# Performance work log

Measured on AMD Instinct MI355X. Metric: run time of the kernel, lower is better.

Reference implementation:

```python
import jax, jax.numpy as jnp
import numpy as np

B, NB, TB = 16, 16, 256          # batch, num cache blocks, tokens per block
EMBED, NH, NKV, HD = 2048, 32, 8, 64  # embed dim, query heads, kv heads, head dim
LAST_OFFSET = 192                # valid length of the final cached block


def setup_inputs() -> dict:
    key = jax.random.key(0)
    ks = jax.random.split(key, 7)
    w = 0.02
    return {
        "x": jax.random.normal(ks[0], (B, 1, EMBED), jnp.float32),
        "blocks_k": jax.random.normal(ks[1], (NB, B, NKV, TB, HD), jnp.float32),
        "blocks_v": jax.random.normal(ks[2], (NB, B, NKV, TB, HD), jnp.float32),
        "Wq": jax.random.normal(ks[3], (EMBED, EMBED), jnp.float32) * w,
        "Wk": jax.random.normal(ks[4], (NKV * HD, EMBED), jnp.float32) * w,
        "Wv": jax.random.normal(ks[5], (NKV * HD, EMBED), jnp.float32) * w,
        "Wo": jax.random.normal(ks[6], (EMBED, EMBED), jnp.float32) * w,
        "last_offset": LAST_OFFSET,
    }


def reference(x, blocks_k, blocks_v, Wq, Wk, Wv, Wo, last_offset):
    # Decode step (T == 1) of GQA MultiHeadAttention with paged/blockwise KV cache.
    Bx, T, C = x.shape                      # T == 1
    nb, _, hkv, tb, hd = blocks_k.shape
    nh = C // hd
    g = nh // hkv                           # GQA group size
    scale = hd ** -0.5

    # Projections (nn.Linear with bias=False => x @ W.T)
    q = (x @ Wq.T).reshape(Bx, hkv, g, hd)          # (B, H_kv, g, D); T==1 folded
    k_cur = (x @ Wk.T).reshape(Bx, hkv, 1, hd)      # (B, H_kv, 1, D)
    v_cur = (x @ Wv.T).reshape(Bx, hkv, 1, hd)

    # Gather cached blocks into a contiguous view: (nb,B,Hkv,tb,D) -> (B,Hkv,nb*tb,D)
    Kc = jnp.transpose(blocks_k, (1, 2, 0, 3, 4)).reshape(Bx, hkv, nb * tb, hd)
    Vc = jnp.transpose(blocks_v, (1, 2, 0, 3, 4)).reshape(Bx, hkv, nb * tb, hd)
    K = jnp.concatenate([Kc, k_cur], axis=2)        # (B, H_kv, nb*tb+1, D)
    V = jnp.concatenate([Vc, v_cur], axis=2)

    # Valid positions: all full blocks, last cached block truncated to last_offset,
    # plus the current token. Equivalent to the streaming softmax over blocks.
    pos = jnp.arange(nb * tb)
    mask = jnp.concatenate([pos < (nb - 1) * tb + last_offset,
                            jnp.ones((1,), dtype=bool)])

    # GQA scores without materializing expanded KV heads
    scores = jnp.einsum('bhgd,bhkd->bhgk', q, K) * scale   # (B, H_kv, g, L)
    scores = jnp.where(mask, scores, jnp.finfo(scores.dtype).min)
    probs = jax.nn.softmax(scores, axis=-1)
    o = jnp.einsum('bhgk,bhkd->bhgd', probs, V)             # (B, H_kv, g, D)

    atten = o.reshape(Bx, 1, C)                              # heads -> channels
    out = atten @ Wo.T                                       # (B, 1, C)
    return out
```

## Files before the change

### kernel.cpp

```cpp
#include <hip/hip_runtime.h>
#include <cstdint>
#include <cstddef>

#define BATCH 16
#define NBLK 16
#define TB 256
#define EMBED 2048
#define NKV 8
#define GQ 4
#define HD 64
#define NQROWS 3072
#define TTOT 4096
#define QSCALE 0.18033688011112042f
#define NEGBIG (-1e30f)

#define OFF_PARTM  49152
#define OFF_PARTS  81920
#define OFF_CMB    114688
#define OFF_PARTO  116736
#define OFF_ATTEN  641024
#define OFF_S      673792

__device__ __forceinline__ float dot4(float4 a, float4 b) {
  return a.x * b.x + a.y * b.y + a.z * b.z + a.w * b.w;
}

template <int CTRL>
__device__ __forceinline__ float dpp_add(float x) {
  return x + __int_as_float(
                 __builtin_amdgcn_mov_dpp(__float_as_int(x), CTRL, 0xF, 0xF, true));
}

#define PROJ_RPB 4
__global__ __launch_bounds__(256) void proj_kernel(
    const float* __restrict__ x, const float* __restrict__ Wq,
    const float* __restrict__ Wk, const float* __restrict__ Wv,
    float* __restrict__ proj) {
  int tid = threadIdx.x;
  int bb = tid & 15, kc = tid >> 4;
  int row0 = blockIdx.x * PROJ_RPB;
  const float* xp = x + (size_t)bb * EMBED + kc * 128;
  const float* wr[PROJ_RPB];
#pragma unroll
  for (int r = 0; r < PROJ_RPB; ++r) {
    int row = row0 + r;
    wr[r] = (row < 2048 ? Wq + (size_t)row * EMBED
             : row < 2560 ? Wk + (size_t)(row - 2048) * EMBED
                          : Wv + (size_t)(row - 2560) * EMBED) + kc * 128;
  }
  float a[PROJ_RPB] = {0.f, 0.f, 0.f, 0.f};
#pragma unroll
  for (int k = 0; k < 128; k += 8) {
    float4 x0 = *reinterpret_cast<const float4*>(xp + k);
    float4 x1 = *reinterpret_cast<const float4*>(xp + k + 4);
#pragma unroll
    for (int r = 0; r < PROJ_RPB; ++r) {
      float4 w0 = *reinterpret_cast<const float4*>(wr[r] + k);
      float4 w1 = *reinterpret_cast<const float4*>(wr[r] + k + 4);
      a[r] += dot4(w0, x0) + dot4(w1, x1);
    }
  }
  int w = tid >> 6, lane = tid & 63;
  __shared__ float red[4][PROJ_RPB][16];
#pragma unroll
  for (int r = 0; r < PROJ_RPB; ++r) {
    float s = a[r];
    s += __shfl_xor(s, 16);
    s += __shfl_xor(s, 32);
    if (lane < 16) red[w][r][lane] = s;
  }
  __syncthreads();
  if (tid < 16 * PROJ_RPB) {
    int r = tid >> 4, b2 = tid & 15;
    float v = red[0][r][b2] + red[1][r][b2] + red[2][r][b2] + red[3][r][b2];
    proj[(size_t)b2 * NQROWS + row0 + r] = v;
  }
}

__global__ __launch_bounds__(256) void score_kernel(
    const float* __restrict__ blocks_k, const float* __restrict__ proj,
    const int* __restrict__ last_offset, float* __restrict__ sbuf,
    float* __restrict__ part_m, float* __restrict__ part_s) {
  int nb = blockIdx.x, b = blockIdx.y, h = blockIdx.z;
  int tid = threadIdx.x;
  int w = tid >> 6, lane = tid & 63;
  int tq = lane >> 2;
  int qd = lane & 3;
  int valid = (nb == NBLK - 1) ? last_offset[0] : TB;

  float4 qv[GQ][4];
  const float* qbase = proj + (size_t)b * NQROWS + h * GQ * HD + qd * 16;
#pragma unroll
  for (int gi = 0; gi < GQ; ++gi)
#pragma unroll
    for (int j = 0; j < 4; ++j)
      qv[gi][j] = *reinterpret_cast<const float4*>(qbase + gi * HD + j * 4);

  const float* kg = blocks_k + (((size_t)nb * BATCH + b) * NKV + h) * (TB * HD);
  float* sout = sbuf + ((size_t)(b * NKV + h)) * (TTOT * GQ) +
                (size_t)(nb * TB + w * 64) * GQ;

  float m[GQ], sm[GQ];
#pragma unroll
  for (int gi = 0; gi < GQ; ++gi) { m[gi] = NEGBIG; sm[gi] = 0.f; }

#pragma unroll
  for (int i = 0; i < 4; ++i) {
    int tl = w * 64 + i * 16 + tq;
    const float* kp = kg + (size_t)tl * HD + qd * 16;
    float4 k0 = *reinterpret_cast<const float4*>(kp);
    float4 k1 = *reinterpret_cast<const float4*>(kp + 4);
    float4 k2 = *reinterpret_cast<const float4*>(kp + 8);
    float4 k3 = *reinterpret_cast<const float4*>(kp + 12);
    float s[GQ];
#pragma unroll
    for (int gi = 0; gi < GQ; ++gi) {
      s[gi] = dot4(qv[gi][0], k0) + dot4(qv[gi][1], k1) +
              dot4(qv[gi][2], k2) + dot4(qv[gi][3], k3);
      s[gi] = dpp_add<0xB1>(s[gi]);
      s[gi] = dpp_add<0x4E>(s[gi]);
      s[gi] = (tl < valid) ? s[gi] : NEGBIG;
    }
#pragma unroll
    for (int gi = 0; gi < GQ; ++gi) {
      float im = s[gi];
#pragma unroll
      for (int mask = 4; mask < 64; mask <<= 1) im = fmaxf(im, __shfl_xor(im, mask));
      float mn = fmaxf(m[gi], im);
      float c = exp2f((m[gi] - mn) * QSCALE);
      float e = exp2f((s[gi] - mn) * QSCALE);
      float es = e;
#pragma unroll
      for (int mask = 4; mask < 64; mask <<= 1) es += __shfl_xor(es, mask);
      sm[gi] = sm[gi] * c + es;
      m[gi] = mn;
    }
    float v01 = (qd & 1) ? s[1] : s[0];
    float v23 = (qd & 1) ? s[3] : s[2];
    float v = (qd & 2) ? v23 : v01;
    sout[(size_t)(i * 16) * GQ + lane] = v;
  }

  if (lane == 0) {
#pragma unroll
    for (int gi = 0; gi < GQ; ++gi) {
      size_t wi = ((size_t)(b * NKV + h) * GQ + gi);
      part_m[wi * 64 + nb * 4 + w] = m[gi];
      part_s[wi * 64 + nb * 4 + w] = sm[gi];
    }
  }
}

__global__ __launch_bounds__(256) void combine_kernel(
    const float* __restrict__ proj, const float* __restrict__ part_m,
    const float* __restrict__ part_s, float4* __restrict__ cmb) {
  int tid = threadIdx.x;
  int wi = blockIdx.x * 4 + (tid >> 6);
  int lane = tid & 63;
  int b = wi >> 5;
  int h = (wi >> 2) & 7;
  int gi = wi & 3;

  float pm = part_m[(size_t)wi * 64 + lane];
  float ps = part_s[(size_t)wi * 64 + lane];

  float qd = proj[(size_t)b * NQROWS + (h * GQ + gi) * HD + lane];
  float kd = proj[(size_t)b * NQROWS + 2048 + h * HD + lane];
  float sp = qd * kd;
#pragma unroll
  for (int mask = 1; mask < 64; mask <<= 1) sp += __shfl_xor(sp, mask);

  float M = pm;
#pragma unroll
  for (int mask = 1; mask < 64; mask <<= 1) M = fmaxf(M, __shfl_xor(M, mask));
  M = fmaxf(M, sp);

  float contrib = ps * exp2f((pm - M) * QSCALE);
#pragma unroll
  for (int mask = 1; mask < 64; mask <<= 1) contrib += __shfl_xor(contrib, mask);
  float p_cur = exp2f((sp - M) * QSCALE);
  float T = contrib + p_cur;
  if (lane == 0) cmb[wi] = make_float4(M, p_cur, 1.f / T, 0.f);
}

__global__ __launch_bounds__(256) void pv_kernel(
    const float* __restrict__ blocks_v, const float* __restrict__ sbuf,
    const float4* __restrict__ cmb, float* __restrict__ part_o) {
  int nb = blockIdx.x, b = blockIdx.y, h = blockIdx.z;
  int tid = threadIdx.x;
  int w = tid >> 6, lane = tid & 63;
  int sub = lane >> 4, dl = (lane & 15) * 4;

  const float* vg = blocks_v + (((size_t)nb * BATCH + b) * NKV + h) * (TB * HD);
  const float* sg = sbuf + ((size_t)(b * NKV + h)) * (TTOT * GQ) +
                    (size_t)(nb * TB) * GQ;

  float Mv[GQ];
#pragma unroll
  for (int gi = 0; gi < GQ; ++gi)
    Mv[gi] = cmb[(size_t)(b * NKV + h) * GQ + gi].x;

  float4 acc[GQ];
#pragma unroll
  for (int gi = 0; gi < GQ; ++gi) acc[gi] = make_float4(0.f, 0.f, 0.f, 0.f);

#pragma unroll
  for (int i = 0; i < 4; ++i) {
    float4 v4[4], s4[4];
#pragma unroll
    for (int j = 0; j < 4; ++j) {
      int tl = w * 64 + i * 16 + j * 4 + sub;
      v4[j] = *reinterpret_cast<const float4*>(vg + (size_t)tl * HD + dl);
      s4[j] = *reinterpret_cast<const float4*>(sg + (size_t)tl * GQ);
    }
#pragma unroll
    for (int j = 0; j < 4; ++j) {
      float p0 = exp2f((s4[j].x - Mv[0]) * QSCALE);
      float p1 = exp2f((s4[j].y - Mv[1]) * QSCALE);
      float p2 = exp2f((s4[j].z - Mv[2]) * QSCALE);
      float p3 = exp2f((s4[j].w - Mv[3]) * QSCALE);
      acc[0].x += p0 * v4[j].x; acc[0].y += p0 * v4[j].y;
      acc[0].z += p0 * v4[j].z; acc[0].w += p0 * v4[j].w;
      acc[1].x += p1 * v4[j].x; acc[1].y += p1 * v4[j].y;
      acc[1].z += p1 * v4[j].z; acc[1].w += p1 * v4[j].w;
      acc[2].x += p2 * v4[j].x; acc[2].y += p2 * v4[j].y;
      acc[2].z += p2 * v4[j].z; acc[2].w += p2 * v4[j].w;
      acc[3].x += p3 * v4[j].x; acc[3].y += p3 * v4[j].y;
      acc[3].z += p3 * v4[j].z; acc[3].w += p3 * v4[j].w;
    }
  }

#pragma unroll
  for (int mask = 16; mask <= 32; mask <<= 1) {
#pragma unroll
    for (int gi = 0; gi < GQ; ++gi) {
      acc[gi].x += __shfl_xor(acc[gi].x, mask);
      acc[gi].y += __shfl_xor(acc[gi].y, mask);
      acc[gi].z += __shfl_xor(acc[gi].z, mask);
      acc[gi].w += __shfl_xor(acc[gi].w, mask);
    }
  }

  __shared__ float lds_o[4][GQ][HD];
  if (lane < 16) {
#pragma unroll
    for (int gi = 0; gi < GQ; ++gi)
      *reinterpret_cast<float4*>(&lds_o[w][gi][dl]) = acc[gi];
  }
  __syncthreads();
  if (w == 0) {
    int d = lane;
#pragma unroll
    for (int gi = 0; gi < GQ; ++gi) {
      float o = lds_o[0][gi][d] + lds_o[1][gi][d] + lds_o[2][gi][d] + lds_o[3][gi][d];
      part_o[(((size_t)(b * NKV + h) * GQ + gi) * NBLK + nb) * HD + d] = o;
    }
  }
}

__global__ __launch_bounds__(256) void reduce_kernel(
    const float* __restrict__ proj, const float* __restrict__ part_o,
    const float4* __restrict__ cmb, float* __restrict__ atten) {
  int tid = threadIdx.x;
  int wi = blockIdx.x * 4 + (tid >> 6);
  int lane = tid & 63;
  int b = wi >> 5;
  int h = (wi >> 2) & 7;
  int gi = wi & 3;
  size_t pidx = (size_t)wi * NBLK;

  float4 c4 = cmb[wi];
  float vd = proj[(size_t)b * NQROWS + 2560 + h * HD + lane];
  float o = c4.y * vd;
#pragma unroll
  for (int nb = 0; nb < NBLK; ++nb) o += part_o[(pidx + nb) * HD + lane];
  atten[(size_t)b * EMBED + (h * GQ + gi) * HD + lane] = o * c4.z;
}

#define OUT_RPB 4
__global__ __launch_bounds__(256) void out_kernel(
    const float* __restrict__ atten, const float* __restrict__ Wo,
    float* __restrict__ out) {
  int tid = threadIdx.x;
  int bb = tid & 15, kc = tid >> 4;
  int row0 = blockIdx.x * OUT_RPB;
  const float* xp = atten + (size_t)bb * EMBED + kc * 128;
  float a[OUT_RPB] = {0.f, 0.f, 0.f, 0.f};
#pragma unroll
  for (int k = 0; k < 128; k += 8) {
    float4 x0 = *reinterpret_cast<const float4*>(xp + k);
    float4 x1 = *reinterpret_cast<const float4*>(xp + k + 4);
#pragma unroll
    for (int r = 0; r < OUT_RPB; ++r) {
      const float* wp = Wo + (size_t)(row0 + r) * EMBED + kc * 128;
      float4 w0 = *reinterpret_cast<const float4*>(wp + k);
      float4 w1 = *reinterpret_cast<const float4*>(wp + k + 4);
      a[r] += dot4(w0, x0) + dot4(w1, x1);
    }
  }
  int w = tid >> 6, lane = tid & 63;
  __shared__ float red[4][OUT_RPB][16];
#pragma unroll
  for (int r = 0; r < OUT_RPB; ++r) {
    float s = a[r];
    s += __shfl_xor(s, 16);
    s += __shfl_xor(s, 32);
    if (lane < 16) red[w][r][lane] = s;
  }
  __syncthreads();
  if (tid < 16 * OUT_RPB) {
    int r = tid >> 4, b2 = tid & 15;
    float v = red[0][r][b2] + red[1][r][b2] + red[2][r][b2] + red[3][r][b2];
    out[(size_t)b2 * EMBED + row0 + r] = v;
  }
}

extern "C" void kernel_launch(void* const* d_in, const int* in_sizes, int n_in,
                              void* d_out, int out_size, void* d_ws, size_t ws_size,
                              hipStream_t stream) {
  const float* x = (const float*)d_in[0];
  const float* bk = (const float*)d_in[1];
  const float* bv = (const float*)d_in[2];
  const float* Wq = (const float*)d_in[3];
  const float* Wk = (const float*)d_in[4];
  const float* Wv = (const float*)d_in[5];
  const float* Wo = (const float*)d_in[6];
  const int* lo = (const int*)d_in[7];

  float* ws = (float*)d_ws;
  float* proj = ws;
  float* part_m = ws + OFF_PARTM;
  float* part_s = ws + OFF_PARTS;
  float4* cmb = (float4*)(ws + OFF_CMB);
  float* part_o = ws + OFF_PARTO;
  float* atten = ws + OFF_ATTEN;
  float* sbuf = ws + OFF_S;
  float* out = (float*)d_out;

  proj_kernel<<<NQROWS / PROJ_RPB, 256, 0, stream>>>(x, Wq, Wk, Wv, proj);
  score_kernel<<<dim3(NBLK, BATCH, NKV), 256, 0, stream>>>(bk, proj, lo, sbuf,
                                                           part_m, part_s);
  combine_kernel<<<(BATCH * NKV * GQ) / 4, 256, 0, stream>>>(proj, part_m,
                                                             part_s, cmb);
  pv_kernel<<<dim3(NBLK, BATCH, NKV), 256, 0, stream>>>(bv, sbuf, cmb, part_o);
  reduce_kernel<<<(BATCH * NKV * GQ) / 4, 256, 0, stream>>>(proj, part_o, cmb,
                                                            atten);
  out_kernel<<<EMBED / OUT_RPB, 256, 0, stream>>>(atten, Wo, out);
}
```

Measured before the change: 141.6 us.

## Split each KV block across two workgroups and batch loads upfront

The score and PV kernels now launch twice as many workgroups, each covering half of a 256-token cache block. Each wave handles 32 tokens and issues all of its K/V and score loads before a sched_barrier, which gives more memory parallelism per wave. The score kernel drops the per-iteration online-softmax rescaling and computes one max/sum per wave. The partial max/sum and partial output buffers double in size, so the combine and reduce kernels read and sum twice as many partials, and the workspace offsets grow to fit.

```diff
diff --git a/kernel.cpp b/kernel.cpp
--- a/kernel.cpp
+++ b/kernel.cpp
@@ -15,11 +15,11 @@
 #define NEGBIG (-1e30f)
 
 #define OFF_PARTM  49152
-#define OFF_PARTS  81920
-#define OFF_CMB    114688
-#define OFF_PARTO  116736
-#define OFF_ATTEN  641024
-#define OFF_S      673792
+#define OFF_PARTS  114688
+#define OFF_CMB    180224
+#define OFF_PARTO  182272
+#define OFF_ATTEN  1230848
+#define OFF_S      1263616
 
 __device__ __forceinline__ float dot4(float4 a, float4 b) {
   return a.x * b.x + a.y * b.y + a.z * b.z + a.w * b.w;
@@ -81,12 +81,14 @@
     const float* __restrict__ blocks_k, const float* __restrict__ proj,
     const int* __restrict__ last_offset, float* __restrict__ sbuf,
     float* __restrict__ part_m, float* __restrict__ part_s) {
-  int nb = blockIdx.x, b = blockIdx.y, h = blockIdx.z;
+  int tb2 = blockIdx.x, b = blockIdx.y, h = blockIdx.z;
+  int nb = tb2 >> 1;
   int tid = threadIdx.x;
   int w = tid >> 6, lane = tid & 63;
   int tq = lane >> 2;
   int qd = lane & 3;
   int valid = (nb == NBLK - 1) ? last_offset[0] : TB;
+  int tok0 = (tb2 & 1) * 128 + w * 32;
 
   float4 qv[GQ][4];
   const float* qbase = proj + (size_t)b * NQROWS + h * GQ * HD + qd * 16;
@@ -97,56 +99,52 @@
       qv[gi][j] = *reinterpret_cast<const float4*>(qbase + gi * HD + j * 4);
 
   const float* kg = blocks_k + (((size_t)nb * BATCH + b) * NKV + h) * (TB * HD);
+
+  float4 kr[2][4];
+#pragma unroll
+  for (int i = 0; i < 2; ++i) {
+    const float* kp = kg + (size_t)(tok0 + i * 16 + tq) * HD + qd * 16;
+#pragma unroll
+    for (int j = 0; j < 4; ++j)
+      kr[i][j] = *reinterpret_cast<const float4*>(kp + j * 4);
+  }
+  __builtin_amdgcn_sched_barrier(0);
+
+  float s[2][GQ];
+#pragma unroll
+  for (int i = 0; i < 2; ++i) {
+#pragma unroll
+    for (int gi = 0; gi < GQ; ++gi) {
+      float t = dot4(qv[gi][0], kr[i][0]) + dot4(qv[gi][1], kr[i][1]) +
+                dot4(qv[gi][2], kr[i][2]) + dot4(qv[gi][3], kr[i][3]);
+      t = dpp_add<0xB1>(t);
+      t = dpp_add<0x4E>(t);
+      s[i][gi] = (tok0 + i * 16 + tq) < valid ? t : NEGBIG;
+    }
+  }
+
   float* sout = sbuf + ((size_t)(b * NKV + h)) * (TTOT * GQ) +
-                (size_t)(nb * TB + w * 64) * GQ;
-
-  float m[GQ], sm[GQ];
-#pragma unroll
-  for (int gi = 0; gi < GQ; ++gi) { m[gi] = NEGBIG; sm[gi] = 0.f; }
-
-#pragma unroll
-  for (int i = 0; i < 4; ++i) {
-    int tl = w * 64 + i * 16 + tq;
-    const float* kp = kg + (size_t)tl * HD + qd * 16;
-    float4 k0 = *reinterpret_cast<const float4*>(kp);
-    float4 k1 = *reinterpret_cast<const float4*>(kp + 4);
-    float4 k2 = *reinterpret_cast<const float4*>(kp + 8);
-    float4 k3 = *reinterpret_cast<const float4*>(kp + 12);
-    float s[GQ];
-#pragma unroll
-    for (int gi = 0; gi < GQ; ++gi) {
-      s[gi] = dot4(qv[gi][0], k0) + dot4(qv[gi][1], k1) +
-              dot4(qv[gi][2], k2) + dot4(qv[gi][3], k3);
-      s[gi] = dpp_add<0xB1>(s[gi]);
-      s[gi] = dpp_add<0x4E>(s[gi]);
-      s[gi] = (tl < valid) ? s[gi] : NEGBIG;
-    }
-#pragma unroll
-    for (int gi = 0; gi < GQ; ++gi) {
-      float im = s[gi];
-#pragma unroll
-      for (int mask = 4; mask < 64; mask <<= 1) im = fmaxf(im, __shfl_xor(im, mask));
-      float mn = fmaxf(m[gi], im);
-      float c = exp2f((m[gi] - mn) * QSCALE);
-      float e = exp2f((s[gi] - mn) * QSCALE);
-      float es = e;
-#pragma unroll
-      for (int mask = 4; mask < 64; mask <<= 1) es += __shfl_xor(es, mask);
-      sm[gi] = sm[gi] * c + es;
-      m[gi] = mn;
-    }
-    float v01 = (qd & 1) ? s[1] : s[0];
-    float v23 = (qd & 1) ? s[3] : s[2];
-    float v = (qd & 2) ? v23 : v01;
-    sout[(size_t)(i * 16) * GQ + lane] = v;
-  }
-
-  if (lane == 0) {
-#pragma unroll
-    for (int gi = 0; gi < GQ; ++gi) {
-      size_t wi = ((size_t)(b * NKV + h) * GQ + gi);
-      part_m[wi * 64 + nb * 4 + w] = m[gi];
-      part_s[wi * 64 + nb * 4 + w] = sm[gi];
+                (size_t)(nb * TB + tok0) * GQ;
+#pragma unroll
+  for (int i = 0; i < 2; ++i) {
+    float v01 = (qd & 1) ? s[i][1] : s[i][0];
+    float v23 = (qd & 1) ? s[i][3] : s[i][2];
+    sout[(size_t)(i * 16) * GQ + lane] = (qd & 2) ? v23 : v01;
+  }
+
+#pragma unroll
+  for (int gi = 0; gi < GQ; ++gi) {
+    float mx = fmaxf(s[0][gi], s[1][gi]);
+#pragma unroll
+    for (int mask = 4; mask < 64; mask <<= 1)
+      mx = fmaxf(mx, __shfl_xor(mx, mask));
+    float sm = exp2f((s[0][gi] - mx) * QSCALE) + exp2f((s[1][gi] - mx) * QSCALE);
+#pragma unroll
+    for (int mask = 4; mask < 64; mask <<= 1) sm += __shfl_xor(sm, mask);
+    if (lane == 0) {
+      size_t wi = (size_t)(b * NKV + h) * GQ + gi;
+      part_m[wi * 128 + tb2 * 4 + w] = mx;
+      part_s[wi * 128 + tb2 * 4 + w] = sm;
     }
   }
 }
@@ -161,8 +159,10 @@
   int h = (wi >> 2) & 7;
   int gi = wi & 3;
 
-  float pm = part_m[(size_t)wi * 64 + lane];
-  float ps = part_s[(size_t)wi * 64 + lane];
+  float pm_a = part_m[(size_t)wi * 128 + lane];
+  float pm_b = part_m[(size_t)wi * 128 + 64 + lane];
+  float ps_a = part_s[(size_t)wi * 128 + lane];
+  float ps_b = part_s[(size_t)wi * 128 + 64 + lane];
 
   float qd = proj[(size_t)b * NQROWS + (h * GQ + gi) * HD + lane];
   float kd = proj[(size_t)b * NQROWS + 2048 + h * HD + lane];
@@ -170,64 +170,66 @@
 #pragma unroll
   for (int mask = 1; mask < 64; mask <<= 1) sp += __shfl_xor(sp, mask);
 
-  float M = pm;
+  float M = fmaxf(pm_a, pm_b);
 #pragma unroll
   for (int mask = 1; mask < 64; mask <<= 1) M = fmaxf(M, __shfl_xor(M, mask));
   M = fmaxf(M, sp);
 
-  float contrib = ps * exp2f((pm - M) * QSCALE);
+  float contrib = ps_a * exp2f((pm_a - M) * QSCALE) +
+                  ps_b * exp2f((pm_b - M) * QSCALE);
 #pragma unroll
   for (int mask = 1; mask < 64; mask <<= 1) contrib += __shfl_xor(contrib, mask);
   float p_cur = exp2f((sp - M) * QSCALE);
-  float T = contrib + p_cur;
-  if (lane == 0) cmb[wi] = make_float4(M, p_cur, 1.f / T, 0.f);
+  if (lane == 0) cmb[wi] = make_float4(M, p_cur, 1.f / (contrib + p_cur), 0.f);
 }
 
 __global__ __launch_bounds__(256) void pv_kernel(
     const float* __restrict__ blocks_v, const float* __restrict__ sbuf,
     const float4* __restrict__ cmb, float* __restrict__ part_o) {
-  int nb = blockIdx.x, b = blockIdx.y, h = blockIdx.z;
+  int tb2 = blockIdx.x, b = blockIdx.y, h = blockIdx.z;
+  int nb = tb2 >> 1;
   int tid = threadIdx.x;
   int w = tid >> 6, lane = tid & 63;
   int sub = lane >> 4, dl = (lane & 15) * 4;
+  int tok0 = (tb2 & 1) * 128 + w * 32;
 
   const float* vg = blocks_v + (((size_t)nb * BATCH + b) * NKV + h) * (TB * HD);
   const float* sg = sbuf + ((size_t)(b * NKV + h)) * (TTOT * GQ) +
-                    (size_t)(nb * TB) * GQ;
+                    (size_t)(nb * TB + tok0) * GQ;
 
   float Mv[GQ];
 #pragma unroll
   for (int gi = 0; gi < GQ; ++gi)
     Mv[gi] = cmb[(size_t)(b * NKV + h) * GQ + gi].x;
 
+  float4 vr[8], sr[8];
+#pragma unroll
+  for (int i = 0; i < 8; ++i)
+    vr[i] = *reinterpret_cast<const float4*>(
+        vg + (size_t)(tok0 + i * 4 + sub) * HD + dl);
+#pragma unroll
+  for (int i = 0; i < 8; ++i)
+    sr[i] = *reinterpret_cast<const float4*>(sg + (size_t)(i * 4 + sub) * GQ);
+  __builtin_amdgcn_sched_barrier(0);
+
   float4 acc[GQ];
 #pragma unroll
   for (int gi = 0; gi < GQ; ++gi) acc[gi] = make_float4(0.f, 0.f, 0.f, 0.f);
 
 #pragma unroll
-  for (int i = 0; i < 4; ++i) {
-    float4 v4[4], s4[4];
-#pragma unroll
-    for (int j = 0; j < 4; ++j) {
-      int tl = w * 64 + i * 16 + j * 4 + sub;
-      v4[j] = *reinterpret_cast<const float4*>(vg + (size_t)tl * HD + dl);
-      s4[j] = *reinterpret_cast<const float4*>(sg + (size_t)tl * GQ);
-    }
-#pragma unroll
-    for (int j = 0; j < 4; ++j) {
-      float p0 = exp2f((s4[j].x - Mv[0]) * QSCALE);
-      float p1 = exp2f((s4[j].y - Mv[1]) * QSCALE);
-      float p2 = exp2f((s4[j].z - Mv[2]) * QSCALE);
-      float p3 = exp2f((s4[j].w - Mv[3]) * QSCALE);
-      acc[0].x += p0 * v4[j].x; acc[0].y += p0 * v4[j].y;
-      acc[0].z += p0 * v4[j].z; acc[0].w += p0 * v4[j].w;
-      acc[1].x += p1 * v4[j].x; acc[1].y += p1 * v4[j].y;
-      acc[1].z += p1 * v4[j].z; acc[1].w += p1 * v4[j].w;
-      acc[2].x += p2 * v4[j].x; acc[2].y += p2 * v4[j].y;
-      acc[2].z += p2 * v4[j].z; acc[2].w += p2 * v4[j].w;
-      acc[3].x += p3 * v4[j].x; acc[3].y += p3 * v4[j].y;
-      acc[3].z += p3 * v4[j].z; acc[3].w += p3 * v4[j].w;
-    }
+  for (int i = 0; i < 8; ++i) {
+    float p0 = exp2f((sr[i].x - Mv[0]) * QSCALE);
+    float p1 = exp2f((sr[i].y - Mv[1]) * QSCALE);
+    float p2 = exp2f((sr[i].z - Mv[2]) * QSCALE);
+    float p3 = exp2f((sr[i].w - Mv[3]) * QSCALE);
+    acc[0].x += p0 * vr[i].x; acc[0].y += p0 * vr[i].y;
+    acc[0].z += p0 * vr[i].z; acc[0].w += p0 * vr[i].w;
+    acc[1].x += p1 * vr[i].x; acc[1].y += p1 * vr[i].y;
+    acc[1].z += p1 * vr[i].z; acc[1].w += p1 * vr[i].w;
+    acc[2].x += p2 * vr[i].x; acc[2].y += p2 * vr[i].y;
+    acc[2].z += p2 * vr[i].z; acc[2].w += p2 * vr[i].w;
+    acc[3].x += p3 * vr[i].x; acc[3].y += p3 * vr[i].y;
+    acc[3].z += p3 * vr[i].z; acc[3].w += p3 * vr[i].w;
   }
 
 #pragma unroll
@@ -253,7 +255,7 @@
 #pragma unroll
     for (int gi = 0; gi < GQ; ++gi) {
       float o = lds_o[0][gi][d] + lds_o[1][gi][d] + lds_o[2][gi][d] + lds_o[3][gi][d];
-      part_o[(((size_t)(b * NKV + h) * GQ + gi) * NBLK + nb) * HD + d] = o;
+      part_o[(((size_t)(b * NKV + h) * GQ + gi) * 32 + tb2) * HD + d] = o;
     }
   }
 }
@@ -267,13 +269,13 @@
   int b = wi >> 5;
   int h = (wi >> 2) & 7;
   int gi = wi & 3;
-  size_t pidx = (size_t)wi * NBLK;
+  size_t pidx = (size_t)wi * 32;
 
   float4 c4 = cmb[wi];
   float vd = proj[(size_t)b * NQROWS + 2560 + h * HD + lane];
   float o = c4.y * vd;
 #pragma unroll
-  for (int nb = 0; nb < NBLK; ++nb) o += part_o[(pidx + nb) * HD + lane];
+  for (int s2 = 0; s2 < 32; ++s2) o += part_o[(pidx + s2) * HD + lane];
   atten[(size_t)b * EMBED + (h * GQ + gi) * HD + lane] = o * c4.z;
 }
 
@@ -338,11 +340,11 @@
   float* out = (float*)d_out;
 
   proj_kernel<<<NQROWS / PROJ_RPB, 256, 0, stream>>>(x, Wq, Wk, Wv, proj);
-  score_kernel<<<dim3(NBLK, BATCH, NKV), 256, 0, stream>>>(bk, proj, lo, sbuf,
-                                                           part_m, part_s);
+  score_kernel<<<dim3(32, BATCH, NKV), 256, 0, stream>>>(bk, proj, lo, sbuf,
+                                                         part_m, part_s);
   combine_kernel<<<(BATCH * NKV * GQ) / 4, 256, 0, stream>>>(proj, part_m,
                                                              part_s, cmb);
-  pv_kernel<<<dim3(NBLK, BATCH, NKV), 256, 0, stream>>>(bv, sbuf, cmb, part_o);
+  pv_kernel<<<dim3(32, BATCH, NKV), 256, 0, stream>>>(bv, sbuf, cmb, part_o);
   reduce_kernel<<<(BATCH * NKV * GQ) / 4, 256, 0, stream>>>(proj, part_o, cmb,
                                                             atten);
   out_kernel<<<EMBED / OUT_RPB, 256, 0, stream>>>(atten, Wo, out);
```

Measured after the change: 142.6 us. About the same (+0.7%).
